# Kernel optimization log

Hardware: AMD Instinct MI355X
Metric: run time of the kernel (lower is better)

Reference implementation:

```python
import jax, jax.numpy as jnp
import numpy as np

ELEM, EMBD = 512, 512

def setup_inputs() -> dict:
    key = jax.random.key(0)
    ks = jax.random.split(key, 7)
    s = 1.0 / np.sqrt(ELEM)
    return {
        "x": jax.random.normal(ks[0], (8, 2048, ELEM), dtype=jnp.float32),
        "Wq": jax.random.normal(ks[1], (ELEM, EMBD), dtype=jnp.float32) * s,
        "bq": jnp.zeros((EMBD,), dtype=jnp.float32),
        "Wk": jax.random.normal(ks[2], (ELEM, EMBD), dtype=jnp.float32) * s,
        "bk": jnp.zeros((EMBD,), dtype=jnp.float32),
        "Wv": jax.random.normal(ks[3], (ELEM, EMBD), dtype=jnp.float32) * s,
        "bv": jnp.zeros((EMBD,), dtype=jnp.float32),
    }

def reference(x, Wq, bq, Wk, bk, Wv, bv):
    # x: [N, S, E]
    q = x @ Wq + bq            # [N, S, D]
    k = x @ Wk + bk            # [N, S, D]
    v = x @ Wv + bv            # [N, S, D]
    # NOTE: original has no 1/sqrt(d) scaling.
    logits = jnp.einsum('nsd,ntd->nst', q, k)   # [N, S, S]
    attn = jax.nn.softmax(logits, axis=-1)
    return jnp.einsum('nst,ntd->nsd', attn, v)  # [N, S, D]
```

## Files before the change

kernel.cpp:

```cpp
#include <hip/hip_runtime.h>
#include <hip/hip_fp16.h>

#define SEQ 2048
#define DIM 512

typedef __attribute__((ext_vector_type(8))) short short8;
typedef __attribute__((ext_vector_type(4))) float f32x4;
typedef _Float16 h8 __attribute__((ext_vector_type(8)));
typedef _Float16 h4 __attribute__((ext_vector_type(4)));

#define MFMA16(a, b, c) __builtin_amdgcn_mfma_f32_16x16x32_f16((a), (b), (c), 0, 0, 0)

#define GLOAD_LDS16(g, l)                                                              \
    __builtin_amdgcn_global_load_lds(                                                  \
        (const __attribute__((address_space(1))) unsigned int*)(g),                    \
        (__attribute__((address_space(3))) unsigned int*)(l), 16, 0, 0)

template <int MODE>
__global__ __launch_bounds__(512, 1) void gemmw(
    const _Float16* __restrict__ A, const _Float16* __restrict__ B,
    const float* __restrict__ biasA, const float* __restrict__ biasB,
    _Float16* __restrict__ o0, _Float16* __restrict__ ovt) {
    extern __shared__ char sm[];
    constexpr int T  = (MODE == 0) ? 16 : 8;
    constexpr int PA = 512;
    constexpr int PB = (MODE == 0) ? 1024 : 512;

    int tid = threadIdx.x, wid = tid >> 6, lane = tid & 63, r = lane & 15, g = lane >> 4;
    int wm = wid >> 1, wn = wid & 1;
    int m0 = blockIdx.x * 256, n0 = blockIdx.y * 128;

    const _Float16* Ab = A + (size_t)m0 * 512;
    const _Float16* Bb = B + (size_t)n0 * PB;

    const char* gA[4];
    const char* gB[2];
    int ldsA[4], ldsB[2];
#pragma unroll
    for (int j = 0; j < 4; ++j) {
        int ci = j * 512 + tid;
        int row = ci >> 3, cl = ci & 7;
        int col16 = cl ^ (row & 7);
        gA[j] = (const char*)Ab + (size_t)row * (PA * 2) + col16 * 16;
        ldsA[j] = ci * 16;
    }
#pragma unroll
    for (int j = 0; j < 2; ++j) {
        int ci = j * 512 + tid;
        int row = ci >> 3, cl = ci & 7;
        int col16 = cl ^ (row & 7);
        gB[j] = (const char*)Bb + (size_t)row * (PB * 2) + col16 * 16;
        ldsB[j] = ci * 16;
    }
    int offA[4][2], offB[4][2];
#pragma unroll
    for (int m = 0; m < 4; ++m) {
        int rowA = wm * 64 + m * 16 + r;
        int rowB = wn * 64 + m * 16 + r;
#pragma unroll
        for (int ks = 0; ks < 2; ++ks) {
            offA[m][ks] = rowA * 128 + (((ks * 4 + g) ^ (rowA & 7)) * 16);
            offB[m][ks] = rowB * 128 + (((ks * 4 + g) ^ (rowB & 7)) * 16);
        }
    }

    f32x4 acc[4][4];
#pragma unroll
    for (int m = 0; m < 4; ++m)
#pragma unroll
        for (int n = 0; n < 4; ++n) acc[m][n] = (f32x4)(0.0f);

    auto STG = [&](int t, int b) {
        int ka = (MODE == 0) ? ((t & 7) * 128) : (t * 128);
        int kb = t * 128;
        char* dA = sm + b * 49152;
        char* dB = sm + b * 49152 + 32768;
#pragma unroll
        for (int j = 0; j < 4; ++j) GLOAD_LDS16(gA[j] + ka, dA + ldsA[j]);
#pragma unroll
        for (int j = 0; j < 2; ++j) GLOAD_LDS16(gB[j] + kb, dB + ldsB[j]);
    };

    STG(0, 0);
    STG(1, 1);
    asm volatile("s_waitcnt vmcnt(6)" ::: "memory");
    __builtin_amdgcn_s_barrier();

#pragma unroll
    for (int t = 0; t < T; ++t) {
        const int buf = t % 3;
        if (t + 2 < T) STG(t + 2, (t + 2) % 3);
        const char* bA = sm + buf * 49152;
        const char* bB = sm + buf * 49152 + 32768;
        h8 af[4][2], bf[4][2];
#pragma unroll
        for (int m = 0; m < 4; ++m)
#pragma unroll
            for (int ks = 0; ks < 2; ++ks) {
                af[m][ks] = *(const h8*)(bA + offA[m][ks]);
                bf[m][ks] = *(const h8*)(bB + offB[m][ks]);
            }
        __builtin_amdgcn_s_setprio(1);
#pragma unroll
        for (int ks = 0; ks < 2; ++ks)
#pragma unroll
            for (int m = 0; m < 4; ++m)
#pragma unroll
                for (int n = 0; n < 4; ++n)
                    acc[m][n] = MFMA16(af[m][ks], bf[n][ks], acc[m][n]);
        __builtin_amdgcn_s_setprio(0);
        if (t + 2 < T) asm volatile("s_waitcnt vmcnt(6)" ::: "memory");
        else if (t + 1 < T) asm volatile("s_waitcnt vmcnt(0)" ::: "memory");
        if (t + 1 < T) __builtin_amdgcn_s_barrier();
    }

    if (MODE == 0) {
#pragma unroll
        for (int n = 0; n < 4; ++n) {
            int col = n0 + wn * 64 + n * 16 + r;
            float bi = biasA[col];
#pragma unroll
            for (int m = 0; m < 4; ++m) {
                int grow0 = m0 + wm * 64 + m * 16 + 4 * g;
                for (int reg = 0; reg < 4; ++reg)
                    o0[(size_t)(grow0 + reg) * 512 + col] =
                        (_Float16)(acc[m][n][reg] + bi);
            }
        }
    } else {
        int p = n0 >> 9, ncl = n0 & 511;
        if (p == 0) {
#pragma unroll
            for (int n = 0; n < 4; ++n) {
                int col = ncl + wn * 64 + n * 16 + r;
                float bi = biasA[col];
#pragma unroll
                for (int m = 0; m < 4; ++m) {
                    int grow0 = m0 + wm * 64 + m * 16 + 4 * g;
                    for (int reg = 0; reg < 4; ++reg)
                        o0[(size_t)(grow0 + reg) * 512 + col] =
                            (_Float16)(acc[m][n][reg] + bi);
                }
            }
        } else {
            __syncthreads();
            _Float16* tt = (_Float16*)sm;
#pragma unroll
            for (int n = 0; n < 4; ++n) {
                int dloc = wn * 64 + n * 16 + r;
                float bi = biasB[ncl + dloc];
#pragma unroll
                for (int m = 0; m < 4; ++m) {
                    int sloc = wm * 64 + m * 16 + 4 * g;
                    h4 pv;
                    pv[0] = (_Float16)(acc[m][n][0] + bi);
                    pv[1] = (_Float16)(acc[m][n][1] + bi);
                    pv[2] = (_Float16)(acc[m][n][2] + bi);
                    pv[3] = (_Float16)(acc[m][n][3] + bi);
                    *(h4*)(&tt[dloc * 264 + sloc]) = pv;
                }
            }
            __syncthreads();
            int b = m0 >> 11, s0b = m0 & 2047;
            int drow = tid >> 2, part = tid & 3;
            const char* src = (const char*)(tt + drow * 264 + part * 64);
            char* dst = (char*)(ovt + (size_t)b * (512 * 2048) +
                                (size_t)(ncl + drow) * 2048 + s0b + part * 64);
#pragma unroll
            for (int j = 0; j < 8; ++j)
                *(short8*)(dst + j * 16) = *(const short8*)(src + j * 16);
        }
    }
}

template <int MODE>
__global__ __launch_bounds__(256) void gemmn(
    const _Float16* __restrict__ A, const _Float16* __restrict__ B,
    _Float16* __restrict__ ph, float* __restrict__ tmx, float* __restrict__ tsm,
    const float* __restrict__ scb, float* __restrict__ of, int bat0) {
    __shared__ char sm[2 * 32768];
    constexpr int T  = (MODE == 1) ? 8 : 32;
    constexpr int PA = (MODE == 1) ? 512 : 2048;
    constexpr int PB = (MODE == 1) ? 512 : 2048;

    int tid = threadIdx.x, wid = tid >> 6, lane = tid & 63, r = lane & 15, g = lane >> 4;
    int mw = wid >> 1, nw = wid & 1;
    int m0 = blockIdx.x * 128, n0 = blockIdx.y * 128, bz = blockIdx.z;

    const _Float16 *Ab, *Bb;
    if (MODE == 1) {
        int b = bat0 + bz;
        Ab = A + ((size_t)(b * SEQ) + m0) * 512;
        Bb = B + ((size_t)(b * SEQ) + n0) * 512;
    } else {
        int b = bat0 + bz;
        Ab = A + (size_t)bz * (SEQ * (size_t)SEQ) + (size_t)m0 * 2048;
        Bb = B + (size_t)b * (512 * SEQ) + (size_t)n0 * 2048;
    }

    const char* gA[4];
    const char* gB[4];
    int ldsw[4];
#pragma unroll
    for (int j = 0; j < 4; ++j) {
        int ci = (j * 4 + wid) * 64 + lane;
        int row = ci >> 3, cl = ci & 7;
        int col16 = cl ^ (row & 7);
        gA[j] = (const char*)Ab + (size_t)row * (PA * 2) + col16 * 16;
        gB[j] = (const char*)Bb + (size_t)row * (PB * 2) + col16 * 16;
        ldsw[j] = (j * 4 + wid) * 1024;
    }
    int offA[4][2], offB[4][2];
#pragma unroll
    for (int m = 0; m < 4; ++m) {
        int rowA = mw * 64 + m * 16 + r;
        int rowB = nw * 64 + m * 16 + r;
#pragma unroll
        for (int ks = 0; ks < 2; ++ks) {
            offA[m][ks] = rowA * 128 + (((ks * 4 + g) ^ (rowA & 7)) * 16);
            offB[m][ks] = rowB * 128 + (((ks * 4 + g) ^ (rowB & 7)) * 16);
        }
    }
    const float* scp = nullptr;
    if constexpr (MODE == 2)
        scp = scb + (size_t)bz * (32 * SEQ) + m0 + mw * 64 + r;

    f32x4 acc[4][4];
#pragma unroll
    for (int m = 0; m < 4; ++m)
#pragma unroll
        for (int n = 0; n < 4; ++n) acc[m][n] = (f32x4)(0.0f);

    auto STG = [&](int t, int b) {
        int ka = t * 128, kb = t * 128;
        char* dA = sm + b * 32768;
        char* dB = sm + b * 32768 + 16384;
#pragma unroll
        for (int j = 0; j < 4; ++j) {
            GLOAD_LDS16(gA[j] + ka, dA + ldsw[j]);
            GLOAD_LDS16(gB[j] + kb, dB + ldsw[j]);
        }
    };

    STG(0, 0);
    asm volatile("s_waitcnt vmcnt(0)" ::: "memory");
    __builtin_amdgcn_s_barrier();

#pragma unroll
    for (int t = 0; t < T; ++t) {
        const int buf = t & 1;
        if (t + 1 < T) STG(t + 1, buf ^ 1);
        const char* bA = sm + buf * 32768;
        const char* bB = sm + buf * 32768 + 16384;
        h8 af[4][2], bf[4][2];
#pragma unroll
        for (int m = 0; m < 4; ++m)
#pragma unroll
            for (int ks = 0; ks < 2; ++ks) {
                af[m][ks] = *(const h8*)(bA + offA[m][ks]);
                bf[m][ks] = *(const h8*)(bB + offB[m][ks]);
            }
        if constexpr (MODE == 2) {
#pragma unroll
            for (int m = 0; m < 4; ++m) {
                _Float16 s = (_Float16)scp[(size_t)t * SEQ + m * 16];
#pragma unroll
                for (int ks = 0; ks < 2; ++ks)
#pragma unroll
                    for (int j = 0; j < 8; ++j) af[m][ks][j] *= s;
            }
        }
#pragma unroll
        for (int ks = 0; ks < 2; ++ks)
#pragma unroll
            for (int m = 0; m < 4; ++m)
#pragma unroll
                for (int n = 0; n < 4; ++n)
                    acc[m][n] = MFMA16(af[m][ks], bf[n][ks], acc[m][n]);
        if (t + 1 < T) {
            asm volatile("s_waitcnt vmcnt(0)" ::: "memory");
            __builtin_amdgcn_s_barrier();
        }
    }

    if constexpr (MODE == 1) {
        _Float16* pb = ph + (size_t)bz * (SEQ * (size_t)SEQ);
        float* mxp = tmx + (size_t)bz * (32 * SEQ);
        float* smp = tsm + (size_t)bz * (32 * SEQ);
        int tileIdx = (n0 + nw * 64) >> 6;
#pragma unroll
        for (int m = 0; m < 4; ++m)
#pragma unroll
            for (int reg = 0; reg < 4; ++reg) {
                int row = m0 + mw * 64 + m * 16 + 4 * g + reg;
                float v0 = acc[m][0][reg], v1 = acc[m][1][reg];
                float v2 = acc[m][2][reg], v3 = acc[m][3][reg];
                float tm = fmaxf(fmaxf(v0, v1), fmaxf(v2, v3));
                for (int d = 1; d < 16; d <<= 1) tm = fmaxf(tm, __shfl_xor(tm, d));
                float p0 = __expf(v0 - tm), p1 = __expf(v1 - tm);
                float p2 = __expf(v2 - tm), p3 = __expf(v3 - tm);
                float s = (p0 + p1) + (p2 + p3);
                for (int d = 1; d < 16; d <<= 1) s += __shfl_xor(s, d);
                size_t rb = (size_t)row * SEQ + n0 + nw * 64;
                pb[rb + 0 * 16 + r] = (_Float16)p0;
                pb[rb + 1 * 16 + r] = (_Float16)p1;
                pb[rb + 2 * 16 + r] = (_Float16)p2;
                pb[rb + 3 * 16 + r] = (_Float16)p3;
                if (r == 0) {
                    mxp[tileIdx * SEQ + row] = tm;
                    smp[tileIdx * SEQ + row] = s;
                }
            }
    } else {
        int b = bat0 + bz;
#pragma unroll
        for (int n = 0; n < 4; ++n) {
            int col = n0 + nw * 64 + n * 16 + r;
#pragma unroll
            for (int m = 0; m < 4; ++m) {
                int grow0 = m0 + mw * 64 + m * 16 + 4 * g;
                for (int reg = 0; reg < 4; ++reg)
                    of[(size_t)(b * SEQ + grow0 + reg) * 512 + col] = acc[m][n][reg];
            }
        }
    }
}

__global__ __launch_bounds__(256) void k3lite(
    const float* __restrict__ tmx, const float* __restrict__ tsm,
    float* __restrict__ sc) {
    int row = blockIdx.x * 256 + threadIdx.x;
    int bz = row >> 11, rr = row & 2047;
    const float* mx = tmx + (size_t)bz * (32 * SEQ);
    const float* sp = tsm + (size_t)bz * (32 * SEQ);
    float* so = sc + (size_t)bz * (32 * SEQ);
    float mv[32];
    float m = -3.0e38f;
#pragma unroll
    for (int t = 0; t < 32; ++t) {
        mv[t] = mx[t * SEQ + rr];
        m = fmaxf(m, mv[t]);
    }
    float cv[32];
    float l = 0.0f;
#pragma unroll
    for (int t = 0; t < 32; ++t) {
        cv[t] = __expf(mv[t] - m);
        l += cv[t] * sp[t * SEQ + rr];
    }
    float inv = 1.0f / l;
#pragma unroll
    for (int t = 0; t < 32; ++t) so[t * SEQ + rr] = cv[t] * inv;
}

__global__ __launch_bounds__(256) void k0a_splitw(
    const float* __restrict__ Wq, const float* __restrict__ Wk, const float* __restrict__ Wv,
    _Float16* __restrict__ wq, _Float16* __restrict__ wkv) {
    int idx = blockIdx.x * 256 + threadIdx.x;
    int p = idx >> 18;
    int rem = idx & 262143;
    int k = rem >> 9, n = rem & 511;
    if (p == 0) {
        float w = Wq[rem];
        _Float16 h = (_Float16)w;
        wq[(size_t)n * 1024 + k] = h;
        wq[(size_t)n * 1024 + 512 + k] = (_Float16)(w - (float)h);
    } else if (p == 1) {
        wkv[(size_t)n * 512 + k] = (_Float16)Wk[rem];
    } else {
        wkv[(size_t)(512 + n) * 512 + k] = (_Float16)Wv[rem];
    }
}

__global__ __launch_bounds__(256) void k0b_splitx(
    const float* __restrict__ x, _Float16* __restrict__ xh) {
    size_t i = (size_t)(blockIdx.x * 256 + threadIdx.x) * 4;
    float4 v = *(const float4*)(x + i);
    h4 h;
    h[0] = (_Float16)v.x; h[1] = (_Float16)v.y;
    h[2] = (_Float16)v.z; h[3] = (_Float16)v.w;
    *(h4*)(xh + i) = h;
}

extern "C" void kernel_launch(void* const* d_in, const int* in_sizes, int n_in,
                              void* d_out, int out_size, void* d_ws, size_t ws_size,
                              hipStream_t stream) {
    const float* x  = (const float*)d_in[0];
    const float* Wq = (const float*)d_in[1];
    const float* bq = (const float*)d_in[2];
    const float* Wk = (const float*)d_in[3];
    const float* bk = (const float*)d_in[4];
    const float* Wv = (const float*)d_in[5];
    const float* bv = (const float*)d_in[6];
    float* out = (float*)d_out;

    char* ws = (char*)d_ws;
    const size_t QSZ = 16777216;
    _Float16* wq  = (_Float16*)(ws);
    _Float16* wkv = (_Float16*)(ws + 1048576);
    _Float16* xh = (_Float16*)(ws + 3145728);
    _Float16* qh = (_Float16*)(ws + 3145728 + 1 * QSZ);
    _Float16* kh = (_Float16*)(ws + 3145728 + 2 * QSZ);
    _Float16* vt = (_Float16*)(ws + 3145728 + 3 * QSZ);
    const size_t sbase = 3145728 + 4 * QSZ;

    const int LDSW = 3 * 49152;
    hipFuncSetAttribute((const void*)gemmw<0>,
                        hipFuncAttributeMaxDynamicSharedMemorySize, LDSW);
    hipFuncSetAttribute((const void*)gemmw<1>,
                        hipFuncAttributeMaxDynamicSharedMemorySize, LDSW);

    k0a_splitw<<<3072, 256, 0, stream>>>(Wq, Wk, Wv, wq, wkv);
    k0b_splitx<<<8192, 256, 0, stream>>>(x, xh);
    gemmw<0><<<dim3(64, 4), 512, LDSW, stream>>>(xh, wq, bq, nullptr, qh, nullptr);
    gemmw<1><<<dim3(64, 8), 512, LDSW, stream>>>(xh, wkv, bk, bv, kh, vt);

    const size_t PSZ = (size_t)SEQ * SEQ * 2;
    const size_t STF = 32 * SEQ;
    const size_t BSZ = PSZ + 3 * STF * 4;
    size_t avail = (ws_size > sbase) ? (ws_size - sbase) : 0;
    int chunk = (int)(avail / BSZ);
    if (chunk < 1) chunk = 1;
    if (chunk > 8) chunk = 8;
    _Float16* pbuf = (_Float16*)(ws + sbase);
    float* tmax = (float*)(ws + sbase + (size_t)chunk * PSZ);
    float* tsum = tmax + (size_t)chunk * STF;
    float* scb  = tsum + (size_t)chunk * STF;

    for (int b0 = 0; b0 < 8; b0 += chunk) {
        int nb = (8 - b0 < chunk) ? (8 - b0) : chunk;
        gemmn<1><<<dim3(16, 16, nb), 256, 0, stream>>>(qh, kh, pbuf, tmax, tsum,
                                                       nullptr, nullptr, b0);
        k3lite<<<dim3(nb * 8), 256, 0, stream>>>(tmax, tsum, scb);
        gemmn<2><<<dim3(16, 4, nb), 256, 0, stream>>>((const _Float16*)pbuf, vt,
                                                      nullptr, nullptr, nullptr,
                                                      scb, out, b0);
    }
}
```

Before: 176.6 us.

## Remap GEMM blocks per XCD and move softmax rescale into separate pass

The two projection GEMMs and the PV GEMM now launch as 1D grids. Block indices are remapped so that consecutive blocks on the same XCD share A-row tiles, which should improve L2 reuse. The per-tile softmax rescaling of P is no longer done inside the PV GEMM's inner loop. A new k3norm kernel rescales P in place before that GEMM. This removes ALU work and scale loads from the GEMM's hot loop, at the cost of an extra read and write pass over the P buffer.

```diff
diff --git a/kernel.cpp b/kernel.cpp
--- a/kernel.cpp
+++ b/kernel.cpp
@@ -28,7 +28,10 @@
 
     int tid = threadIdx.x, wid = tid >> 6, lane = tid & 63, r = lane & 15, g = lane >> 4;
     int wm = wid >> 1, wn = wid & 1;
-    int m0 = blockIdx.x * 256, n0 = blockIdx.y * 128;
+    int L = blockIdx.x, xcd = L & 7, s = L >> 3;
+    int m0, n0;
+    if (MODE == 0) { m0 = (xcd * 8 + (s >> 2)) * 256; n0 = (s & 3) * 128; }
+    else           { m0 = (xcd * 8 + (s >> 3)) * 256; n0 = (s & 7) * 128; }
 
     const _Float16* Ab = A + (size_t)m0 * 512;
     const _Float16* Bb = B + (size_t)n0 * PB;
@@ -177,7 +180,7 @@
 __global__ __launch_bounds__(256) void gemmn(
     const _Float16* __restrict__ A, const _Float16* __restrict__ B,
     _Float16* __restrict__ ph, float* __restrict__ tmx, float* __restrict__ tsm,
-    const float* __restrict__ scb, float* __restrict__ of, int bat0) {
+    float* __restrict__ of, int bat0) {
     __shared__ char sm[2 * 32768];
     constexpr int T  = (MODE == 1) ? 8 : 32;
     constexpr int PA = (MODE == 1) ? 512 : 2048;
@@ -185,7 +188,16 @@
 
     int tid = threadIdx.x, wid = tid >> 6, lane = tid & 63, r = lane & 15, g = lane >> 4;
     int mw = wid >> 1, nw = wid & 1;
-    int m0 = blockIdx.x * 128, n0 = blockIdx.y * 128, bz = blockIdx.z;
+    int m0, n0, bz;
+    if (MODE == 1) {
+        m0 = blockIdx.x * 128; n0 = blockIdx.y * 128; bz = blockIdx.z;
+    } else {
+        int L = blockIdx.x, xcd = L & 7, s = L >> 3;
+        bz = s >> 3;
+        int rem = s & 7;
+        m0 = (xcd * 2 + (rem >> 2)) * 128;
+        n0 = (rem & 3) * 128;
+    }
 
     const _Float16 *Ab, *Bb;
     if (MODE == 1) {
@@ -221,9 +233,6 @@
             offB[m][ks] = rowB * 128 + (((ks * 4 + g) ^ (rowB & 7)) * 16);
         }
     }
-    const float* scp = nullptr;
-    if constexpr (MODE == 2)
-        scp = scb + (size_t)bz * (32 * SEQ) + m0 + mw * 64 + r;
 
     f32x4 acc[4][4];
 #pragma unroll
@@ -260,16 +269,6 @@
                 af[m][ks] = *(const h8*)(bA + offA[m][ks]);
                 bf[m][ks] = *(const h8*)(bB + offB[m][ks]);
             }
-        if constexpr (MODE == 2) {
-#pragma unroll
-            for (int m = 0; m < 4; ++m) {
-                _Float16 s = (_Float16)scp[(size_t)t * SEQ + m * 16];
-#pragma unroll
-                for (int ks = 0; ks < 2; ++ks)
-#pragma unroll
-                    for (int j = 0; j < 8; ++j) af[m][ks][j] *= s;
-            }
-        }
 #pragma unroll
         for (int ks = 0; ks < 2; ++ks)
 #pragma unroll
@@ -353,6 +352,20 @@
     for (int t = 0; t < 32; ++t) so[t * SEQ + rr] = cv[t] * inv;
 }
 
+__global__ __launch_bounds__(256) void k3norm(
+    _Float16* __restrict__ pbuf, const float* __restrict__ scb) {
+    int row = blockIdx.x;
+    int bz = row >> 11, rr = row & 2047;
+    _Float16* pr = pbuf + ((size_t)bz * SEQ + rr) * SEQ;
+    const float* so = scb + (size_t)bz * (32 * SEQ);
+    int j = threadIdx.x;
+    h8 v = *(const h8*)(pr + j * 8);
+    float sc = so[(size_t)(j >> 3) * SEQ + rr];
+#pragma unroll
+    for (int e = 0; e < 8; ++e) v[e] = (_Float16)((float)v[e] * sc);
+    *(h8*)(pr + j * 8) = v;
+}
+
 __global__ __launch_bounds__(256) void k0a_splitw(
     const float* __restrict__ Wq, const float* __restrict__ Wk, const float* __restrict__ Wv,
     _Float16* __restrict__ wq, _Float16* __restrict__ wkv) {
@@ -412,8 +425,8 @@
 
     k0a_splitw<<<3072, 256, 0, stream>>>(Wq, Wk, Wv, wq, wkv);
     k0b_splitx<<<8192, 256, 0, stream>>>(x, xh);
-    gemmw<0><<<dim3(64, 4), 512, LDSW, stream>>>(xh, wq, bq, nullptr, qh, nullptr);
-    gemmw<1><<<dim3(64, 8), 512, LDSW, stream>>>(xh, wkv, bk, bv, kh, vt);
+    gemmw<0><<<256, 512, LDSW, stream>>>(xh, wq, bq, nullptr, qh, nullptr);
+    gemmw<1><<<512, 512, LDSW, stream>>>(xh, wkv, bk, bv, kh, vt);
 
     const size_t PSZ = (size_t)SEQ * SEQ * 2;
     const size_t STF = 32 * SEQ;
@@ -430,10 +443,11 @@
     for (int b0 = 0; b0 < 8; b0 += chunk) {
         int nb = (8 - b0 < chunk) ? (8 - b0) : chunk;
         gemmn<1><<<dim3(16, 16, nb), 256, 0, stream>>>(qh, kh, pbuf, tmax, tsum,
-                                                       nullptr, nullptr, b0);
+                                                       nullptr, b0);
         k3lite<<<dim3(nb * 8), 256, 0, stream>>>(tmax, tsum, scb);
-        gemmn<2><<<dim3(16, 4, nb), 256, 0, stream>>>((const _Float16*)pbuf, vt,
-                                                      nullptr, nullptr, nullptr,
-                                                      scb, out, b0);
-    }
-}
+        k3norm<<<dim3(nb * SEQ), 256, 0, stream>>>(pbuf, scb);
+        gemmn<2><<<dim3(nb * 64), 256, 0, stream>>>((const _Float16*)pbuf, vt,
+                                                    nullptr, nullptr, nullptr,
+                                                    out, b0);
+    }
+}
```

Result: slower. 187.1 us (+6.0%).
